# Performance work log

Measured on AMD Instinct MI355X. Metric: run time of the kernel, lower is better.

Reference implementation:

```python
import jax, jax.numpy as jnp
import numpy as np

N_NODES = 100000
N_EDGES = 1600000
D_IN = 128
D_HID = 64
N_CLASSES = 64


def setup_inputs() -> dict:
    key = jax.random.key(0)
    ks = jax.random.split(key, 12)
    x = jax.random.normal(ks[0], (N_NODES, D_IN), dtype=jnp.float32)
    edge_index = jax.random.randint(ks[1], (2, N_EDGES), 0, N_NODES, dtype=jnp.int64)
    def lin(k, fan_in, fan_out):
        k1, k2 = jax.random.split(k)
        bound = 1.0 / np.sqrt(fan_in)
        w = jax.random.uniform(k1, (fan_in, fan_out), jnp.float32, -bound, bound)
        b = jax.random.uniform(k2, (fan_out,), jnp.float32, -bound, bound)
        return w, b
    w1a, b1a = lin(ks[2], D_IN, D_HID)
    w1b, b1b = lin(ks[3], D_HID, D_HID)
    w2a, b2a = lin(ks[4], D_HID, D_HID)
    w2b, b2b = lin(ks[5], D_HID, N_CLASSES)
    return {"x": x, "edge_index": edge_index,
            "w1a": w1a, "b1a": b1a, "w1b": w1b, "b1b": b1b,
            "w2a": w2a, "b2a": b2a, "w2b": w2b, "b2b": b2b}


def _gin_agg(x, src, dst):
    # GINConv with eps=0: (1+eps)*x_i + sum_{j->i} x_j
    agg = jax.ops.segment_sum(x[src], dst, num_segments=N_NODES)
    return x + agg


def reference(x, edge_index, w1a, b1a, w1b, b1b, w2a, b2a, w2b, b2b):
    src, dst = edge_index[0], edge_index[1]
    # conv1: MLP = Linear -> ReLU -> Linear -> ReLU
    h = _gin_agg(x, src, dst)
    h = jax.nn.relu(h @ w1a + b1a)
    h = jax.nn.relu(h @ w1b + b1b)
    # conv2: MLP = Linear -> ReLU -> Linear
    h = _gin_agg(h, src, dst)
    h = jax.nn.relu(h @ w2a + b2a)
    h = h @ w2b + b2b
    # global add pool over the single graph -> [1, num_classes]
    return jnp.sum(h, axis=0, keepdims=True)
```

## Files before the change

### kernel.cpp

```cpp
#include <hip/hip_runtime.h>

#define N_NODES 100000
#define N_EDGES 1600000
#define D_IN 128
#define D 64
#define NBS ((N_NODES + 255) / 256)

__device__ __forceinline__ float bf2f(unsigned short u) {
    union { unsigned int i; float f; } q; q.i = ((unsigned int)u) << 16; return q.f;
}
__device__ __forceinline__ unsigned short f2bf(float f) {
    unsigned int u = __float_as_uint(f);
    unsigned int r = (u + 0x7FFFu + ((u >> 16) & 1u)) >> 16;
    return (unsigned short)r;
}
__device__ __forceinline__ void acc4(float4& a, ushort4 v) {
    a.x += bf2f(v.x); a.y += bf2f(v.y); a.z += bf2f(v.z); a.w += bf2f(v.w);
}


__global__ void k_hist(const int* __restrict__ dst, int* __restrict__ deg) {
    int e = blockIdx.x * 256 + threadIdx.x;
    if (e < N_EDGES) atomicAdd(&deg[dst[e]], 1);
}

__global__ void k_scan1(const int* __restrict__ deg, int* __restrict__ bsum) {
    __shared__ int s[256];
    int t = threadIdx.x;
    int i = blockIdx.x * 256 + t;
    s[t] = (i < N_NODES) ? deg[i] : 0;
    __syncthreads();
    for (int o = 128; o > 0; o >>= 1) {
        if (t < o) s[t] += s[t + o];
        __syncthreads();
    }
    if (t == 0) bsum[blockIdx.x] = s[0];
}

__global__ void k_scan2(const int* __restrict__ bsum, int* __restrict__ boff) {
    __shared__ int s[512];
    int t = threadIdx.x;
    int v = (t < NBS) ? bsum[t] : 0;
    s[t] = v;
    __syncthreads();
    for (int o = 1; o < 512; o <<= 1) {
        int x = (t >= o) ? s[t - o] : 0;
        __syncthreads();
        s[t] += x;
        __syncthreads();
    }
    if (t < NBS) boff[t] = s[t] - v;
}

__global__ void k_scan3(int* __restrict__ offs, const int* __restrict__ boff,
                        int* __restrict__ cursor) {
    __shared__ int s[256];
    int t = threadIdx.x;
    int i = blockIdx.x * 256 + t;
    int v = (i < N_NODES) ? offs[i] : 0;
    s[t] = v;
    __syncthreads();
    for (int o = 1; o < 256; o <<= 1) {
        int x = (t >= o) ? s[t - o] : 0;
        __syncthreads();
        s[t] += x;
        __syncthreads();
    }
    int off = boff[blockIdx.x] + s[t] - v;
    if (i < N_NODES) {
        offs[i] = off;
        cursor[i] = off;
        if (i == N_NODES - 1) offs[N_NODES] = off + v;
    }
}

__global__ void k_fill(const int* __restrict__ src, const int* __restrict__ dst,
                       int* __restrict__ cursor, int* __restrict__ csr) {
    int e = blockIdx.x * 256 + threadIdx.x;
    if (e < N_EDGES) {
        int d = dst[e];
        int p = atomicAdd(&cursor[d], 1);
        csr[p] = src[e];
    }
}

__global__ __launch_bounds__(256) void k_gemm1(const float* __restrict__ x,
                                               const float* __restrict__ w,
                                               unsigned short* __restrict__ z) {
    __shared__ float ws[D_IN][D];
    __shared__ float xs[16][D_IN + 1];
    int t = threadIdx.x;
    {
        const float4* w4 = (const float4*)w;
        float4* s4 = (float4*)&ws[0][0];
        for (int i = t; i < (D_IN * D) / 4; i += 256) s4[i] = w4[i];
    }
    int r = t >> 4, c = t & 15;
    __syncthreads();
    for (int base = blockIdx.x * 16; base < N_NODES; base += gridDim.x * 16) {
        for (int i = t; i < 16 * (D_IN / 4); i += 256) {
            int row = i >> 5, k4 = i & 31;
            float4 v = ((const float4*)(x + (size_t)(base + row) * D_IN))[k4];
            xs[row][k4 * 4 + 0] = v.x; xs[row][k4 * 4 + 1] = v.y;
            xs[row][k4 * 4 + 2] = v.z; xs[row][k4 * 4 + 3] = v.w;
        }
        __syncthreads();
        float4 acc = {0.f, 0.f, 0.f, 0.f};
        for (int k = 0; k < D_IN; k++) {
            float xv = xs[r][k];
            float4 wv = *(const float4*)&ws[k][c * 4];
            acc.x += xv * wv.x; acc.y += xv * wv.y;
            acc.z += xv * wv.z; acc.w += xv * wv.w;
        }
        ushort4 p;
        p.x = f2bf(acc.x); p.y = f2bf(acc.y); p.z = f2bf(acc.z); p.w = f2bf(acc.w);
        *(ushort4*)(z + (size_t)(base + r) * D + c * 4) = p;
        __syncthreads();
    }
}

__global__ __launch_bounds__(256, 6) void k_conv1(const unsigned short* __restrict__ z,
                                                  const int* __restrict__ offs,
                                                  const int* __restrict__ csr,
                                                  const float* __restrict__ b1a,
                                                  const float* __restrict__ w1b,
                                                  const float* __restrict__ b1b,
                                                  const float* __restrict__ w2a,
                                                  unsigned short* __restrict__ u) {
    __shared__ unsigned short w1s[D][D];
    __shared__ unsigned short w2s[D][D];
    __shared__ float h1s[16][D + 1];
    __shared__ float h2s[16][D + 1];
    int t = threadIdx.x;
    int r = t >> 4, c = t & 15;
    {
        for (int i = t; i < (D * D) / 4; i += 256) {
            float4 a = ((const float4*)w1b)[i];
            ushort4 p; p.x = f2bf(a.x); p.y = f2bf(a.y); p.z = f2bf(a.z); p.w = f2bf(a.w);
            *(ushort4*)&(&w1s[0][0])[i * 4] = p;
            float4 b = ((const float4*)w2a)[i];
            ushort4 q; q.x = f2bf(b.x); q.y = f2bf(b.y); q.z = f2bf(b.z); q.w = f2bf(b.w);
            *(ushort4*)&(&w2s[0][0])[i * 4] = q;
        }
    }
    float4 vb1a = ((const float4*)b1a)[c];
    float4 vb1b = ((const float4*)b1b)[c];
    __syncthreads();

    const size_t c4 = (size_t)(c * 4);
    for (int base = blockIdx.x * 16; base < N_NODES; base += gridDim.x * 16) {
        int node = base + r;
        float4 acc = {vb1a.x, vb1a.y, vb1a.z, vb1a.w};
        acc4(acc, *(const ushort4*)(z + (size_t)node * D + c4));
        int e0 = offs[node], e1 = offs[node + 1];
        int e = e0;
        for (; e + 8 <= e1; e += 8) {
            int s0 = csr[e + 0], s1 = csr[e + 1], s2 = csr[e + 2], s3 = csr[e + 3];
            int s4 = csr[e + 4], s5 = csr[e + 5], s6 = csr[e + 6], s7 = csr[e + 7];
            ushort4 v0 = *(const ushort4*)(z + (size_t)s0 * D + c4);
            ushort4 v1 = *(const ushort4*)(z + (size_t)s1 * D + c4);
            ushort4 v2 = *(const ushort4*)(z + (size_t)s2 * D + c4);
            ushort4 v3 = *(const ushort4*)(z + (size_t)s3 * D + c4);
            ushort4 v4 = *(const ushort4*)(z + (size_t)s4 * D + c4);
            ushort4 v5 = *(const ushort4*)(z + (size_t)s5 * D + c4);
            ushort4 v6 = *(const ushort4*)(z + (size_t)s6 * D + c4);
            ushort4 v7 = *(const ushort4*)(z + (size_t)s7 * D + c4);
            acc4(acc, v0); acc4(acc, v1); acc4(acc, v2); acc4(acc, v3);
            acc4(acc, v4); acc4(acc, v5); acc4(acc, v6); acc4(acc, v7);
        }
        for (; e < e1; e++) {
            int s = csr[e];
            acc4(acc, *(const ushort4*)(z + (size_t)s * D + c4));
        }
        h1s[r][c * 4 + 0] = fmaxf(acc.x, 0.f);
        h1s[r][c * 4 + 1] = fmaxf(acc.y, 0.f);
        h1s[r][c * 4 + 2] = fmaxf(acc.z, 0.f);
        h1s[r][c * 4 + 3] = fmaxf(acc.w, 0.f);
        __syncthreads();
        float4 a2 = vb1b;
        for (int k = 0; k < D; k++) {
            float hv = h1s[r][k];
            ushort4 wv = *(const ushort4*)&w1s[k][c * 4];
            a2.x += hv * bf2f(wv.x); a2.y += hv * bf2f(wv.y);
            a2.z += hv * bf2f(wv.z); a2.w += hv * bf2f(wv.w);
        }
        h2s[r][c * 4 + 0] = fmaxf(a2.x, 0.f);
        h2s[r][c * 4 + 1] = fmaxf(a2.y, 0.f);
        h2s[r][c * 4 + 2] = fmaxf(a2.z, 0.f);
        h2s[r][c * 4 + 3] = fmaxf(a2.w, 0.f);
        __syncthreads();
        float4 a3 = {0.f, 0.f, 0.f, 0.f};
        for (int k = 0; k < D; k++) {
            float hv = h2s[r][k];
            ushort4 wv = *(const ushort4*)&w2s[k][c * 4];
            a3.x += hv * bf2f(wv.x); a3.y += hv * bf2f(wv.y);
            a3.z += hv * bf2f(wv.z); a3.w += hv * bf2f(wv.w);
        }
        ushort4 p;
        p.x = f2bf(a3.x); p.y = f2bf(a3.y); p.z = f2bf(a3.z); p.w = f2bf(a3.w);
        *(ushort4*)(u + (size_t)node * D + c4) = p;
        __syncthreads();
    }
}

__global__ __launch_bounds__(256) void k_conv2(const unsigned short* __restrict__ u,
                                               const int* __restrict__ offs,
                                               const int* __restrict__ csr,
                                               const float* __restrict__ b2a,
                                               float* __restrict__ colsum) {
    __shared__ float red[16][D + 1];
    int t = threadIdx.x;
    int r = t >> 4, c = t & 15;
    float4 vb = ((const float4*)b2a)[c];
    float4 cs = {0.f, 0.f, 0.f, 0.f};
    const size_t c4 = (size_t)(c * 4);
    for (int base = blockIdx.x * 16; base < N_NODES; base += gridDim.x * 16) {
        int node = base + r;
        float4 acc = {vb.x, vb.y, vb.z, vb.w};
        acc4(acc, *(const ushort4*)(u + (size_t)node * D + c4));
        int e0 = offs[node], e1 = offs[node + 1];
        int e = e0;
        for (; e + 8 <= e1; e += 8) {
            int s0 = csr[e + 0], s1 = csr[e + 1], s2 = csr[e + 2], s3 = csr[e + 3];
            int s4 = csr[e + 4], s5 = csr[e + 5], s6 = csr[e + 6], s7 = csr[e + 7];
            ushort4 v0 = *(const ushort4*)(u + (size_t)s0 * D + c4);
            ushort4 v1 = *(const ushort4*)(u + (size_t)s1 * D + c4);
            ushort4 v2 = *(const ushort4*)(u + (size_t)s2 * D + c4);
            ushort4 v3 = *(const ushort4*)(u + (size_t)s3 * D + c4);
            ushort4 v4 = *(const ushort4*)(u + (size_t)s4 * D + c4);
            ushort4 v5 = *(const ushort4*)(u + (size_t)s5 * D + c4);
            ushort4 v6 = *(const ushort4*)(u + (size_t)s6 * D + c4);
            ushort4 v7 = *(const ushort4*)(u + (size_t)s7 * D + c4);
            acc4(acc, v0); acc4(acc, v1); acc4(acc, v2); acc4(acc, v3);
            acc4(acc, v4); acc4(acc, v5); acc4(acc, v6); acc4(acc, v7);
        }
        for (; e < e1; e++) {
            int s = csr[e];
            acc4(acc, *(const ushort4*)(u + (size_t)s * D + c4));
        }
        cs.x += fmaxf(acc.x, 0.f); cs.y += fmaxf(acc.y, 0.f);
        cs.z += fmaxf(acc.z, 0.f); cs.w += fmaxf(acc.w, 0.f);
    }
    red[r][c * 4 + 0] = cs.x; red[r][c * 4 + 1] = cs.y;
    red[r][c * 4 + 2] = cs.z; red[r][c * 4 + 3] = cs.w;
    __syncthreads();
    if (r == 0) {
        float4 tot = {0.f, 0.f, 0.f, 0.f};
        for (int rr = 0; rr < 16; rr++) {
            tot.x += red[rr][c * 4 + 0]; tot.y += red[rr][c * 4 + 1];
            tot.z += red[rr][c * 4 + 2]; tot.w += red[rr][c * 4 + 3];
        }
        atomicAdd(&colsum[c * 4 + 0], tot.x);
        atomicAdd(&colsum[c * 4 + 1], tot.y);
        atomicAdd(&colsum[c * 4 + 2], tot.z);
        atomicAdd(&colsum[c * 4 + 3], tot.w);
    }
}

__global__ void k_final(const float* __restrict__ colsum, const float* __restrict__ w2b,
                        const float* __restrict__ b2b, float* __restrict__ out) {
    int j = threadIdx.x;
    float acc = (float)N_NODES * b2b[j];
    for (int k = 0; k < D; k++) acc += colsum[k] * w2b[k * D + j];
    out[j] = acc;
}


extern "C" void kernel_launch(void* const* d_in, const int* in_sizes, int n_in,
                              void* d_out, int out_size, void* d_ws, size_t ws_size,
                              hipStream_t stream) {
    const float* x   = (const float*)d_in[0];
    const int*   ei  = (const int*)d_in[1];
    const float* w1a = (const float*)d_in[2];
    const float* b1a = (const float*)d_in[3];
    const float* w1b = (const float*)d_in[4];
    const float* b1b = (const float*)d_in[5];
    const float* w2a = (const float*)d_in[6];
    const float* b2a = (const float*)d_in[7];
    const float* w2b = (const float*)d_in[8];
    const float* b2b = (const float*)d_in[9];
    float* out = (float*)d_out;

    const int* srcp = ei;
    const int* dstp = ei + N_EDGES;

    char* ws = (char*)d_ws;
    unsigned short* z = (unsigned short*)(ws + 0);
    unsigned short* u = (unsigned short*)(ws + 12800000);
    int*   offs   = (int*)(ws + 25600000);
    int*   cursor = (int*)(ws + 26000128);
    int*   csr    = (int*)(ws + 26400128);
    int*   bsum   = (int*)(ws + 32800128);
    int*   boff   = (int*)(ws + 32801920);
    float* colsum = (float*)(ws + 32803712);

    hipMemsetAsync(offs, 0, (N_NODES + 1) * sizeof(int), stream);
    hipMemsetAsync(colsum, 0, D * sizeof(float), stream);

    k_hist <<<(N_EDGES + 255) / 256, 256, 0, stream>>>(dstp, offs);
    k_scan1<<<NBS, 256, 0, stream>>>(offs, bsum);
    k_scan2<<<1, 512, 0, stream>>>(bsum, boff);
    k_scan3<<<NBS, 256, 0, stream>>>(offs, boff, cursor);
    k_fill <<<(N_EDGES + 255) / 256, 256, 0, stream>>>(srcp, dstp, cursor, csr);

    k_gemm1<<<2048, 256, 0, stream>>>(x, w1a, z);
    k_conv1<<<2048, 256, 0, stream>>>(z, offs, csr, b1a, w1b, b1b, w2a, u);
    k_conv2<<<2048, 256, 0, stream>>>(u, offs, csr, b2a, colsum);
    k_final<<<1, 64, 0, stream>>>(colsum, w2b, b2b, out);
}
```

Baseline: 546.6 us.

## Build CSR via two-level bucketed counting sort and widen gather unroll to 16

Replaces the global-atomic histogram, three-pass scan and atomic fill with a two-level counting sort. Edges are first bucketed by dst>>8 using shared-memory histograms and a single-block scan, then each 256-node bucket builds its offsets and CSR entries with shared atomics. This targets the contention and scattered writes of global atomics and makes CSR order within a bucket more local. The neighbour gather in both conv kernels now uses a 16-wide predicated unroll for more memory parallelism, at the cost of more registers and wasted loads on short rows. The single-block scan over about 391K entries is serial per thread and may become a bottleneck.

```diff
diff --git a/kernel.cpp b/kernel.cpp
--- a/kernel.cpp
+++ b/kernel.cpp
@@ -4,7 +4,11 @@
 #define N_EDGES 1600000
 #define D_IN 128
 #define D 64
-#define NBS ((N_NODES + 255) / 256)
+
+#define NBLK 1000
+#define EPB  1600
+#define NB2  391
+#define SCAN_T 1024
 
 __device__ __forceinline__ float bf2f(unsigned short u) {
     union { unsigned int i; float f; } q; q.i = ((unsigned int)u) << 16; return q.f;
@@ -19,45 +23,71 @@
 }
 
 
-__global__ void k_hist(const int* __restrict__ dst, int* __restrict__ deg) {
-    int e = blockIdx.x * 256 + threadIdx.x;
-    if (e < N_EDGES) atomicAdd(&deg[dst[e]], 1);
-}
-
-__global__ void k_scan1(const int* __restrict__ deg, int* __restrict__ bsum) {
+__global__ __launch_bounds__(256) void k_hist1(const int* __restrict__ dst,
+                                               int* __restrict__ bh) {
+    __shared__ int h[NB2];
+    int t = threadIdx.x;
+    for (int i = t; i < NB2; i += 256) h[i] = 0;
+    __syncthreads();
+    int base = blockIdx.x * EPB;
+    for (int i = t; i < EPB; i += 256) atomicAdd(&h[dst[base + i] >> 8], 1);
+    __syncthreads();
+    for (int i = t; i < NB2; i += 256) bh[i * NBLK + blockIdx.x] = h[i];
+}
+
+__global__ __launch_bounds__(SCAN_T) void k_scan(int* __restrict__ bh) {
+    __shared__ int s[SCAN_T];
+    int t = threadIdx.x;
+    const int M = NB2 * NBLK;
+    const int C = (M + SCAN_T - 1) / SCAN_T;
+    int lo = t * C, hi = lo + C; if (hi > M) hi = M;
+    int sum = 0;
+    for (int i = lo; i < hi; i++) sum += bh[i];
+    s[t] = sum;
+    __syncthreads();
+    for (int o = 1; o < SCAN_T; o <<= 1) {
+        int v = (t >= o) ? s[t - o] : 0;
+        __syncthreads();
+        s[t] += v;
+        __syncthreads();
+    }
+    int run = (t > 0) ? s[t - 1] : 0;
+    for (int i = lo; i < hi; i++) { int v = bh[i]; bh[i] = run; run += v; }
+}
+
+__global__ __launch_bounds__(256) void k_scatter1(const int* __restrict__ src,
+                                                  const int* __restrict__ dst,
+                                                  const int* __restrict__ bh,
+                                                  uint2* __restrict__ tmp) {
+    __shared__ int cur[NB2];
+    int t = threadIdx.x;
+    for (int i = t; i < NB2; i += 256) cur[i] = bh[i * NBLK + blockIdx.x];
+    __syncthreads();
+    int base = blockIdx.x * EPB;
+    for (int i = t; i < EPB; i += 256) {
+        int d = dst[base + i];
+        int sv = src[base + i];
+        int p = atomicAdd(&cur[d >> 8], 1);
+        tmp[p] = make_uint2((unsigned)d, (unsigned)sv);
+    }
+}
+
+__global__ __launch_bounds__(256) void k_build(const uint2* __restrict__ tmp,
+                                               const int* __restrict__ bh,
+                                               int* __restrict__ offs,
+                                               int* __restrict__ csr) {
+    __shared__ int deg[256];
     __shared__ int s[256];
-    int t = threadIdx.x;
-    int i = blockIdx.x * 256 + t;
-    s[t] = (i < N_NODES) ? deg[i] : 0;
-    __syncthreads();
-    for (int o = 128; o > 0; o >>= 1) {
-        if (t < o) s[t] += s[t + o];
-        __syncthreads();
-    }
-    if (t == 0) bsum[blockIdx.x] = s[0];
-}
-
-__global__ void k_scan2(const int* __restrict__ bsum, int* __restrict__ boff) {
-    __shared__ int s[512];
-    int t = threadIdx.x;
-    int v = (t < NBS) ? bsum[t] : 0;
-    s[t] = v;
-    __syncthreads();
-    for (int o = 1; o < 512; o <<= 1) {
-        int x = (t >= o) ? s[t - o] : 0;
-        __syncthreads();
-        s[t] += x;
-        __syncthreads();
-    }
-    if (t < NBS) boff[t] = s[t] - v;
-}
-
-__global__ void k_scan3(int* __restrict__ offs, const int* __restrict__ boff,
-                        int* __restrict__ cursor) {
-    __shared__ int s[256];
-    int t = threadIdx.x;
-    int i = blockIdx.x * 256 + t;
-    int v = (i < N_NODES) ? offs[i] : 0;
+    __shared__ int cur[256];
+    int b = blockIdx.x;
+    int t = threadIdx.x;
+    int e0 = bh[b * NBLK];
+    int e1 = (b == NB2 - 1) ? N_EDGES : bh[(b + 1) * NBLK];
+    deg[t] = 0;
+    __syncthreads();
+    for (int i = e0 + t; i < e1; i += 256) atomicAdd(&deg[tmp[i].x & 255u], 1);
+    __syncthreads();
+    int v = deg[t];
     s[t] = v;
     __syncthreads();
     for (int o = 1; o < 256; o <<= 1) {
@@ -66,22 +96,17 @@
         s[t] += x;
         __syncthreads();
     }
-    int off = boff[blockIdx.x] + s[t] - v;
-    if (i < N_NODES) {
-        offs[i] = off;
-        cursor[i] = off;
-        if (i == N_NODES - 1) offs[N_NODES] = off + v;
-    }
-}
-
-__global__ void k_fill(const int* __restrict__ src, const int* __restrict__ dst,
-                       int* __restrict__ cursor, int* __restrict__ csr) {
-    int e = blockIdx.x * 256 + threadIdx.x;
-    if (e < N_EDGES) {
-        int d = dst[e];
-        int p = atomicAdd(&cursor[d], 1);
-        csr[p] = src[e];
-    }
+    int start = e0 + s[t] - v;
+    int node = b * 256 + t;
+    if (node < N_NODES) offs[node] = start;
+    cur[t] = start;
+    __syncthreads();
+    for (int i = e0 + t; i < e1; i += 256) {
+        uint2 p = tmp[i];
+        int pos = atomicAdd(&cur[p.x & 255u], 1);
+        csr[pos] = (int)p.y;
+    }
+    if (b == 0 && t == 0) offs[N_NODES] = N_EDGES;
 }
 
 __global__ __launch_bounds__(256) void k_gemm1(const float* __restrict__ x,
@@ -116,6 +141,27 @@
         p.x = f2bf(acc.x); p.y = f2bf(acc.y); p.z = f2bf(acc.z); p.w = f2bf(acc.w);
         *(ushort4*)(z + (size_t)(base + r) * D + c * 4) = p;
         __syncthreads();
+    }
+}
+
+__device__ __forceinline__ void gather16(float4& acc, const unsigned short* __restrict__ zz,
+                                         const int* __restrict__ csr,
+                                         int e0, int e1, size_t c4) {
+    for (int e = e0; e < e1; e += 16) {
+        int idx[16];
+        #pragma unroll
+        for (int k = 0; k < 16; k++) {
+            int ee = e + k;
+            idx[k] = csr[ee < e1 ? ee : e1 - 1];
+        }
+        ushort4 vv[16];
+        #pragma unroll
+        for (int k = 0; k < 16; k++)
+            vv[k] = *(const ushort4*)(zz + (size_t)idx[k] * D + c4);
+        #pragma unroll
+        for (int k = 0; k < 16; k++) {
+            if (e + k < e1) acc4(acc, vv[k]);
+        }
     }
 }
 
@@ -153,25 +199,7 @@
         float4 acc = {vb1a.x, vb1a.y, vb1a.z, vb1a.w};
         acc4(acc, *(const ushort4*)(z + (size_t)node * D + c4));
         int e0 = offs[node], e1 = offs[node + 1];
-        int e = e0;
-        for (; e + 8 <= e1; e += 8) {
-            int s0 = csr[e + 0], s1 = csr[e + 1], s2 = csr[e + 2], s3 = csr[e + 3];
-            int s4 = csr[e + 4], s5 = csr[e + 5], s6 = csr[e + 6], s7 = csr[e + 7];
-            ushort4 v0 = *(const ushort4*)(z + (size_t)s0 * D + c4);
-            ushort4 v1 = *(const ushort4*)(z + (size_t)s1 * D + c4);
-            ushort4 v2 = *(const ushort4*)(z + (size_t)s2 * D + c4);
-            ushort4 v3 = *(const ushort4*)(z + (size_t)s3 * D + c4);
-            ushort4 v4 = *(const ushort4*)(z + (size_t)s4 * D + c4);
-            ushort4 v5 = *(const ushort4*)(z + (size_t)s5 * D + c4);
-            ushort4 v6 = *(const ushort4*)(z + (size_t)s6 * D + c4);
-            ushort4 v7 = *(const ushort4*)(z + (size_t)s7 * D + c4);
-            acc4(acc, v0); acc4(acc, v1); acc4(acc, v2); acc4(acc, v3);
-            acc4(acc, v4); acc4(acc, v5); acc4(acc, v6); acc4(acc, v7);
-        }
-        for (; e < e1; e++) {
-            int s = csr[e];
-            acc4(acc, *(const ushort4*)(z + (size_t)s * D + c4));
-        }
+        gather16(acc, z, csr, e0, e1, c4);
         h1s[r][c * 4 + 0] = fmaxf(acc.x, 0.f);
         h1s[r][c * 4 + 1] = fmaxf(acc.y, 0.f);
         h1s[r][c * 4 + 2] = fmaxf(acc.z, 0.f);
@@ -219,25 +247,7 @@
         float4 acc = {vb.x, vb.y, vb.z, vb.w};
         acc4(acc, *(const ushort4*)(u + (size_t)node * D + c4));
         int e0 = offs[node], e1 = offs[node + 1];
-        int e = e0;
-        for (; e + 8 <= e1; e += 8) {
-            int s0 = csr[e + 0], s1 = csr[e + 1], s2 = csr[e + 2], s3 = csr[e + 3];
-            int s4 = csr[e + 4], s5 = csr[e + 5], s6 = csr[e + 6], s7 = csr[e + 7];
-            ushort4 v0 = *(const ushort4*)(u + (size_t)s0 * D + c4);
-            ushort4 v1 = *(const ushort4*)(u + (size_t)s1 * D + c4);
-            ushort4 v2 = *(const ushort4*)(u + (size_t)s2 * D + c4);
-            ushort4 v3 = *(const ushort4*)(u + (size_t)s3 * D + c4);
-            ushort4 v4 = *(const ushort4*)(u + (size_t)s4 * D + c4);
-            ushort4 v5 = *(const ushort4*)(u + (size_t)s5 * D + c4);
-            ushort4 v6 = *(const ushort4*)(u + (size_t)s6 * D + c4);
-            ushort4 v7 = *(const ushort4*)(u + (size_t)s7 * D + c4);
-            acc4(acc, v0); acc4(acc, v1); acc4(acc, v2); acc4(acc, v3);
-            acc4(acc, v4); acc4(acc, v5); acc4(acc, v6); acc4(acc, v7);
-        }
-        for (; e < e1; e++) {
-            int s = csr[e];
-            acc4(acc, *(const ushort4*)(u + (size_t)s * D + c4));
-        }
+        gather16(acc, u, csr, e0, e1, c4);
         cs.x += fmaxf(acc.x, 0.f); cs.y += fmaxf(acc.y, 0.f);
         cs.z += fmaxf(acc.z, 0.f); cs.w += fmaxf(acc.w, 0.f);
     }
@@ -287,21 +297,18 @@
     char* ws = (char*)d_ws;
     unsigned short* z = (unsigned short*)(ws + 0);
     unsigned short* u = (unsigned short*)(ws + 12800000);
-    int*   offs   = (int*)(ws + 25600000);
-    int*   cursor = (int*)(ws + 26000128);
-    int*   csr    = (int*)(ws + 26400128);
-    int*   bsum   = (int*)(ws + 32800128);
-    int*   boff   = (int*)(ws + 32801920);
-    float* colsum = (float*)(ws + 32803712);
-
-    hipMemsetAsync(offs, 0, (N_NODES + 1) * sizeof(int), stream);
+    uint2* tmp    = (uint2*)(ws + 25600000);
+    int*   csr    = (int*)(ws + 38400000);
+    int*   bh     = (int*)(ws + 44800000);
+    int*   offs   = (int*)(ws + 46364000);
+    float* colsum = (float*)(ws + 46764032);
+
     hipMemsetAsync(colsum, 0, D * sizeof(float), stream);
 
-    k_hist <<<(N_EDGES + 255) / 256, 256, 0, stream>>>(dstp, offs);
-    k_scan1<<<NBS, 256, 0, stream>>>(offs, bsum);
-    k_scan2<<<1, 512, 0, stream>>>(bsum, boff);
-    k_scan3<<<NBS, 256, 0, stream>>>(offs, boff, cursor);
-    k_fill <<<(N_EDGES + 255) / 256, 256, 0, stream>>>(srcp, dstp, cursor, csr);
+    k_hist1   <<<NBLK, 256, 0, stream>>>(dstp, bh);
+    k_scan    <<<1, SCAN_T, 0, stream>>>(bh);
+    k_scatter1<<<NBLK, 256, 0, stream>>>(srcp, dstp, bh, tmp);
+    k_build   <<<NB2, 256, 0, stream>>>(tmp, bh, offs, csr);
 
     k_gemm1<<<2048, 256, 0, stream>>>(x, w1a, z);
     k_conv1<<<2048, 256, 0, stream>>>(z, offs, csr, b1a, w1b, b1b, w2a, u);
```

New measurement: 1.136 ms. 108% more time.
